# Kernel tuning notes

Measured on AMD Instinct MI355X. Metric: run time of the kernel, lower is better.

The kernel has to match this reference:

```python
import jax, jax.numpy as jnp
import numpy as np

B, D, H, NL, DFF, N = 64, 768, 12, 12, 3072, 197
HD = D // H  # 64
SCALE = HD ** -0.5


def setup_inputs() -> dict:
    key = jax.random.key(0)
    ks = iter(jax.random.split(key, 64))
    def rn(shape, s=0.02):
        return jax.random.normal(next(ks), shape, jnp.float32) * s
    inp = {
        'x': jax.random.normal(next(ks), (B, 12, 1000), jnp.float32),
        # PatchEmbed convs (torch Conv1d weight layout OIH)
        'conv1_w': rn((256, 12, 5), 0.1), 'conv1_b': jnp.zeros((256,), jnp.float32),
        'bn1_g': jnp.ones((256,), jnp.float32), 'bn1_b': jnp.zeros((256,), jnp.float32),
        'bn1_m': jnp.zeros((256,), jnp.float32), 'bn1_v': jnp.ones((256,), jnp.float32),
        'conv2_w': rn((768, 256, 5), 0.05), 'conv2_b': jnp.zeros((768,), jnp.float32),
        'bn2_g': jnp.ones((768,), jnp.float32), 'bn2_b': jnp.zeros((768,), jnp.float32),
        'bn2_m': jnp.zeros((768,), jnp.float32), 'bn2_v': jnp.ones((768,), jnp.float32),
        'cls_token': rn((1, 1, D)), 'pos_embed': rn((1, N, D)),
        # 12 transformer blocks, stacked. Linear weights stored [in, out].
        'ln1_g': jnp.ones((NL, D), jnp.float32), 'ln1_b': jnp.zeros((NL, D), jnp.float32),
        'qkv_w': rn((NL, D, 3 * D)),            # qkv_bias=False
        'proj_w': rn((NL, D, D)), 'proj_b': jnp.zeros((NL, D), jnp.float32),
        'ln2_g': jnp.ones((NL, D), jnp.float32), 'ln2_b': jnp.zeros((NL, D), jnp.float32),
        'fc1_w': rn((NL, D, DFF)), 'fc1_b': jnp.zeros((NL, DFF), jnp.float32),
        'fc2_w': rn((NL, DFF, D)), 'fc2_b': jnp.zeros((NL, D), jnp.float32),
        'norm_g': jnp.ones((D,), jnp.float32), 'norm_b': jnp.zeros((D,), jnp.float32),
        # ProjectionHead (nonlinear): Linear(768->768,no bias)+BN, ReLU, Linear(768->512,no bias)+BN
        'p1_w': rn((D, D)),
        'p1bn_g': jnp.ones((D,), jnp.float32), 'p1bn_b': jnp.zeros((D,), jnp.float32),
        'p1bn_m': jnp.zeros((D,), jnp.float32), 'p1bn_v': jnp.ones((D,), jnp.float32),
        'p2_w': rn((D, 512)),
        'p2bn_g': jnp.ones((512,), jnp.float32), 'p2bn_b': jnp.zeros((512,), jnp.float32),
        'p2bn_m': jnp.zeros((512,), jnp.float32), 'p2bn_v': jnp.ones((512,), jnp.float32),
    }
    return inp


def _conv1d(x, w, b, stride):
    y = jax.lax.conv_general_dilated(x, w, (stride,), 'VALID',
                                     dimension_numbers=('NCH', 'OIH', 'NCH'))
    return y + b[None, :, None]


def _bn_c(x, g, b, m, v, eps=1e-5):  # BatchNorm1d eval, channel axis 1 of (B,C,L)
    return (x - m[None, :, None]) * (g[None, :, None] / jnp.sqrt(v[None, :, None] + eps)) + b[None, :, None]


def _bn_f(x, g, b, m, v, eps=1e-5):  # BatchNorm1d eval on (B,F)
    return (x - m) * (g / jnp.sqrt(v + eps)) + b


def _ln(x, g, b, eps=1e-6):
    mu = x.mean(-1, keepdims=True)
    var = jnp.var(x, axis=-1, keepdims=True)
    return (x - mu) * jax.lax.rsqrt(var + eps) * g + b


def reference(x, conv1_w, conv1_b, bn1_g, bn1_b, bn1_m, bn1_v,
              conv2_w, conv2_b, bn2_g, bn2_b, bn2_m, bn2_v,
              cls_token, pos_embed,
              ln1_g, ln1_b, qkv_w, proj_w, proj_b,
              ln2_g, ln2_b, fc1_w, fc1_b, fc2_w, fc2_b,
              norm_g, norm_b,
              p1_w, p1bn_g, p1bn_b, p1bn_m, p1bn_v,
              p2_w, p2bn_g, p2bn_b, p2bn_m, p2bn_v):
    # PatchEmbed: conv -> ReLU -> BN, twice; then (B, 196, 768)
    h = _bn_c(jax.nn.relu(_conv1d(x, conv1_w, conv1_b, 5)), bn1_g, bn1_b, bn1_m, bn1_v)
    h = _bn_c(jax.nn.relu(_conv1d(h, conv2_w, conv2_b, 1)), bn2_g, bn2_b, bn2_m, bn2_v)
    h = jnp.transpose(h, (0, 2, 1))  # [B, 196, D]
    b = h.shape[0]
    tok = jnp.concatenate([jnp.broadcast_to(cls_token, (b, 1, D)), h], axis=1) + pos_embed  # [B, 197, D]

    for i in range(NL):
        y = _ln(tok, ln1_g[i], ln1_b[i])
        qkv = jnp.einsum('bnd,de->bne', y, qkv_w[i]).reshape(b, N, 3, H, HD)
        q, k, v = jnp.moveaxis(qkv, 2, 0)  # each [B, N, H, HD]
        q = jnp.transpose(q, (0, 2, 1, 3)) * SCALE  # [B, H, N, HD]
        k = jnp.transpose(k, (0, 2, 1, 3))
        v = jnp.transpose(v, (0, 2, 1, 3))
        attn = jax.nn.softmax(jnp.einsum('bhnd,bhmd->bhnm', q, k), axis=-1)
        o = jnp.einsum('bhnm,bhmd->bhnd', attn, v)
        o = jnp.transpose(o, (0, 2, 1, 3)).reshape(b, N, D)
        tok = tok + jnp.einsum('bnd,de->bne', o, proj_w[i]) + proj_b[i]
        y = _ln(tok, ln2_g[i], ln2_b[i])
        y = jax.nn.gelu(jnp.einsum('bnd,df->bnf', y, fc1_w[i]) + fc1_b[i], approximate=False)
        tok = tok + jnp.einsum('bnf,fd->bnd', y, fc2_w[i]) + fc2_b[i]

    cls = _ln(tok, norm_g, norm_b)[:, 0]  # global_pool='token'
    z = _bn_f(cls @ p1_w, p1bn_g, p1bn_b, p1bn_m, p1bn_v)
    z = jax.nn.relu(z)
    z = _bn_f(z @ p2_w, p2bn_g, p2bn_b, p2bn_m, p2bn_v)
    return z
```

## Files before the change

kernel.cpp:

```cpp
#include <hip/hip_runtime.h>
#include <hip/hip_bf16.h>

typedef __hip_bfloat16 bf16;
typedef __attribute__((ext_vector_type(8))) short bf16x8;
typedef __attribute__((ext_vector_type(4))) float f32x4;

__device__ __forceinline__ float bf2f(bf16 v) { return __bfloat162float(v); }
__device__ __forceinline__ unsigned short f2bfu(float f) {
    bf16 h = __float2bfloat16(f);
    return __builtin_bit_cast(unsigned short, h);
}

__device__ __forceinline__ void gload16(const void* g, void* lds) {
    __builtin_amdgcn_global_load_lds(
        (const __attribute__((address_space(1))) unsigned int*)g,
        (__attribute__((address_space(3))) unsigned int*)lds, 16, 0, 0);
}

__device__ __forceinline__ float gelu_f(float x) {
    float u = 0.7978845608f * (x + 0.044715f * x * x * x);
    float e = __expf(-2.0f * fabsf(u));
    float th = (1.f - e) / (1.f + e);
    th = u < 0.f ? -th : th;
    return 0.5f * x * (1.f + th);
}

__global__ __launch_bounds__(256)
void conv1_kernel(const float* __restrict__ x, const float* __restrict__ w,
                  const float* __restrict__ bias,
                  const float* __restrict__ g, const float* __restrict__ b,
                  const float* __restrict__ m, const float* __restrict__ v,
                  bf16* __restrict__ h1) {
    int bo = blockIdx.x;
    int bb = bo >> 8, o = bo & 255;
    int l = threadIdx.x;
    if (l >= 200) return;
    const float* wo = w + o * 60;
    const float* xb = x + bb * 12000;
    float acc = bias[o];
#pragma unroll
    for (int i = 0; i < 12; i++)
#pragma unroll
        for (int t = 0; t < 5; t++)
            acc = fmaf(xb[i * 1000 + 5 * l + t], wo[i * 5 + t], acc);
    acc = fmaxf(acc, 0.f);
    float sc = g[o] * rsqrtf(v[o] + 1e-5f);
    acc = (acc - m[o]) * sc + b[o];
    h1[bo * 200 + l] = __float2bfloat16(acc);
}

__global__ __launch_bounds__(256)
void im2col_kernel(const bf16* __restrict__ h1, bf16* __restrict__ A2) {
    int idx = blockIdx.x * 256 + threadIdx.x;
    int row = idx / 1280, c = idx - row * 1280;
    int bb = row / 196, l = row - bb * 196;
    int i = c / 5, t = c - i * 5;
    A2[idx] = h1[(bb * 256 + i) * 200 + l + t];
}

__global__ __launch_bounds__(256)
void add_cls_pos(const float* __restrict__ cls, const float* __restrict__ pos,
                 float* __restrict__ tok) {
    int idx = blockIdx.x * 256 + threadIdx.x;
    int bb = idx / 768, d = idx - bb * 768;
    tok[(size_t)bb * 197 * 768 + d] = cls[d] + pos[d];
}

__global__ __launch_bounds__(256)
void cvt_kernel(const float* __restrict__ in, bf16* __restrict__ out, int n) {
    int idx = blockIdx.x * 256 + threadIdx.x;
    if (idx < n) out[idx] = __float2bfloat16(in[idx]);
}

__global__ __launch_bounds__(256)
void wtrans_layer(const float* __restrict__ qkvw, const float* __restrict__ projw,
                  const float* __restrict__ fc1w, const float* __restrict__ fc2w,
                  bf16* __restrict__ qkvT, bf16* __restrict__ projT,
                  bf16* __restrict__ fc1T, bf16* __restrict__ fc2T) {
    __shared__ float tile[32][33];
    int blk = blockIdx.x;
    const float* in; bf16* out; int Kd, Nd, t0;
    if (blk < 1728)      { in = qkvw; out = qkvT; Kd = 768;  Nd = 2304; t0 = blk; }
    else if (blk < 2304) { in = projw; out = projT; Kd = 768;  Nd = 768;  t0 = blk - 1728; }
    else if (blk < 4608) { in = fc1w; out = fc1T; Kd = 768;  Nd = 3072; t0 = blk - 2304; }
    else                 { in = fc2w; out = fc2T; Kd = 3072; Nd = 768;  t0 = blk - 4608; }
    int ntiles = Nd >> 5;
    int kt = t0 / ntiles, nt = t0 - kt * ntiles;
    int k0 = kt * 32, n0 = nt * 32;
    int tx = threadIdx.x & 31, ty = threadIdx.x >> 5;
#pragma unroll
    for (int j = 0; j < 4; j++)
        tile[ty + 8 * j][tx] = in[(size_t)(k0 + ty + 8 * j) * Nd + n0 + tx];
    __syncthreads();
#pragma unroll
    for (int j = 0; j < 4; j++)
        out[(size_t)(n0 + ty + 8 * j) * Kd + k0 + tx] = __float2bfloat16(tile[tx][ty + 8 * j]);
}

__global__ __launch_bounds__(256)
void wtrans2(const float* __restrict__ in, bf16* __restrict__ out, int Kd, int Nd) {
    __shared__ float tile[32][33];
    int ntiles = Nd >> 5;
    int kt = blockIdx.x / ntiles, nt = blockIdx.x - kt * ntiles;
    int k0 = kt * 32, n0 = nt * 32;
    int tx = threadIdx.x & 31, ty = threadIdx.x >> 5;
#pragma unroll
    for (int j = 0; j < 4; j++)
        tile[ty + 8 * j][tx] = in[(size_t)(k0 + ty + 8 * j) * Nd + n0 + tx];
    __syncthreads();
#pragma unroll
    for (int j = 0; j < 4; j++)
        out[(size_t)(n0 + ty + 8 * j) * Kd + k0 + tx] = __float2bfloat16(tile[tx][ty + 8 * j]);
}

__global__ __launch_bounds__(256)
void ln_kernel(const float* __restrict__ x, bf16* __restrict__ y,
               const float* __restrict__ g, const float* __restrict__ b,
               int nrows, int xstride) {
    int row = blockIdx.x * 4 + (threadIdx.x >> 6);
    if (row >= nrows) return;
    int l = threadIdx.x & 63;
    const float* xr = x + (size_t)row * xstride;
    float4 v0 = *(const float4*)(xr + l * 4);
    float4 v1 = *(const float4*)(xr + 256 + l * 4);
    float4 v2 = *(const float4*)(xr + 512 + l * 4);
    float s1 = 0.f, s2 = 0.f;
    {
        float e;
        e = v0.x; s1 += e; s2 += e * e;  e = v0.y; s1 += e; s2 += e * e;
        e = v0.z; s1 += e; s2 += e * e;  e = v0.w; s1 += e; s2 += e * e;
        e = v1.x; s1 += e; s2 += e * e;  e = v1.y; s1 += e; s2 += e * e;
        e = v1.z; s1 += e; s2 += e * e;  e = v1.w; s1 += e; s2 += e * e;
        e = v2.x; s1 += e; s2 += e * e;  e = v2.y; s1 += e; s2 += e * e;
        e = v2.z; s1 += e; s2 += e * e;  e = v2.w; s1 += e; s2 += e * e;
    }
#pragma unroll
    for (int off = 1; off < 64; off <<= 1) {
        s1 += __shfl_xor(s1, off);
        s2 += __shfl_xor(s2, off);
    }
    float mu = s1 * (1.f / 768.f);
    float rs = rsqrtf(s2 * (1.f / 768.f) - mu * mu + 1e-6f);
    bf16* yr = y + (size_t)row * 768;
#pragma unroll
    for (int sgi = 0; sgi < 3; sgi++) {
        float4 vv = sgi == 0 ? v0 : (sgi == 1 ? v1 : v2);
        float4 gg = *(const float4*)(g + sgi * 256 + l * 4);
        float4 bb = *(const float4*)(b + sgi * 256 + l * 4);
        ushort4 o;
        o.x = f2bfu((vv.x - mu) * rs * gg.x + bb.x);
        o.y = f2bfu((vv.y - mu) * rs * gg.y + bb.y);
        o.z = f2bfu((vv.z - mu) * rs * gg.z + bb.z);
        o.w = f2bfu((vv.w - mu) * rs * gg.w + bb.w);
        *(ushort4*)(yr + sgi * 256 + l * 4) = o;
    }
}

enum { E_BF16 = 0, E_RESID = 1, E_GELU = 2, E_CONV2 = 3, E_HEAD1 = 4, E_HEAD2 = 5 };
#define GEMM_LDS 65536

template<int EPI>
__global__ __launch_bounds__(256)
void gemm2(const bf16* __restrict__ A, const bf16* __restrict__ Bt,
           int M, int N, int K,
           const float* __restrict__ bias,
           bf16* __restrict__ Co, float* __restrict__ tok,
           const float* __restrict__ bng, const float* __restrict__ bnb,
           const float* __restrict__ bnm, const float* __restrict__ bnv,
           const float* __restrict__ pos) {
    extern __shared__ char smem[];
    const int t = threadIdx.x;
    const int l = t & 63, w = t >> 6;
    const int wm = (w >> 1) * 64, wn = (w & 1) * 64;
    const int row0 = blockIdx.y * 128, col0 = blockIdx.x * 128;
    const int lr = l & 15, kg = l >> 4;

    const int srow = w * 8 + (l >> 3);
    const int sc = ((l & 7) ^ (l >> 3)) * 8;
    const int dstoff = w * 1024 + l * 16;

    const f32x4 zero4 = {0.f, 0.f, 0.f, 0.f};
    f32x4 acc[4][4];
#pragma unroll
    for (int i = 0; i < 4; i++)
#pragma unroll
        for (int j = 0; j < 4; j++) acc[i][j] = zero4;

    auto stage = [&](int b, int k0) {
#pragma unroll
        for (int p = 0; p < 4; p++) {
            int r = srow + p * 32;
            int gra = row0 + r; if (gra >= M) gra = M - 1;
            char* base = smem + b * 32768 + p * 4096 + dstoff;
            gload16(A + (size_t)gra * K + k0 + sc, base);
            gload16(Bt + (size_t)(col0 + r) * K + k0 + sc, base + 16384);
        }
    };

    const int nt = K >> 6;
    stage(0, 0);
    asm volatile("s_waitcnt vmcnt(0)" ::: "memory");
    __syncthreads();

    int cur = 0;
    for (int kt = 0; kt < nt; kt++) {
        if (kt + 1 < nt) stage(cur ^ 1, (kt + 1) << 6);
        const char* Ab = smem + cur * 32768;
        const char* Bb = Ab + 16384;
#pragma unroll
        for (int ks = 0; ks < 2; ks++) {
            bf16x8 af[4], bfv[4];
            const int cc = ((ks * 4 + kg) ^ (lr & 7)) * 16;
#pragma unroll
            for (int i = 0; i < 4; i++) {
                af[i]  = *(const bf16x8*)(Ab + (wm + i * 16 + lr) * 128 + cc);
                bfv[i] = *(const bf16x8*)(Bb + (wn + i * 16 + lr) * 128 + cc);
            }
#pragma unroll
            for (int i = 0; i < 4; i++)
#pragma unroll
                for (int j = 0; j < 4; j++)
                    acc[i][j] = __builtin_amdgcn_mfma_f32_16x16x32_bf16(af[i], bfv[j], acc[i][j], 0, 0, 0);
        }
        asm volatile("s_waitcnt vmcnt(0)" ::: "memory");
        __syncthreads();
        cur ^= 1;
    }

    const int rbase = row0 + wm + (kg << 2);
#pragma unroll
    for (int i = 0; i < 4; i++) {
#pragma unroll
        for (int sr = 0; sr < 4; sr++) {
            int r = rbase + i * 16 + sr;
            if (r < M) {
#pragma unroll
                for (int j = 0; j < 4; j++) {
                    int c = col0 + wn + j * 16 + lr;
                    float vv = acc[i][j][sr];
                    if (EPI == E_BF16) {
                        Co[(size_t)r * N + c] = __float2bfloat16(vv);
                    } else if (EPI == E_RESID) {
                        float* p = tok + (size_t)r * N + c;
                        *p += vv + bias[c];
                    } else if (EPI == E_GELU) {
                        Co[(size_t)r * N + c] = __float2bfloat16(gelu_f(vv + bias[c]));
                    } else if (EPI == E_CONV2) {
                        float xx = vv + bias[c];
                        xx = fmaxf(xx, 0.f);
                        float sc2 = bng[c] * rsqrtf(bnv[c] + 1e-5f);
                        xx = (xx - bnm[c]) * sc2 + bnb[c];
                        int bb = r / 196, ll = r - bb * 196;
                        xx += pos[(size_t)(1 + ll) * 768 + c];
                        tok[(size_t)(bb * 197 + 1 + ll) * 768 + c] = xx;
                    } else if (EPI == E_HEAD1) {
                        float sc2 = bng[c] * rsqrtf(bnv[c] + 1e-5f);
                        float xx = (vv - bnm[c]) * sc2 + bnb[c];
                        xx = fmaxf(xx, 0.f);
                        Co[(size_t)r * N + c] = __float2bfloat16(xx);
                    } else {
                        float sc2 = bng[c] * rsqrtf(bnv[c] + 1e-5f);
                        tok[(size_t)r * N + c] = (vv - bnm[c]) * sc2 + bnb[c];
                    }
                }
            }
        }
    }
}

#define ATTN_LDS (208 * 72 * 2 + 64 * 232 * 2 + 4 * 16 * 232 * 2)

__global__ __launch_bounds__(256)
void attn_kernel(const bf16* __restrict__ qkv, bf16* __restrict__ o) {
    extern __shared__ char smem[];
    bf16* Ks = (bf16*)smem;
    bf16* Vt = Ks + 208 * 72;
    bf16* Pl = Vt + 64 * 232;
    const int bh = blockIdx.x, bb = bh / 12, h = bh - bb * 12;
    const int t = threadIdx.x, w = t >> 6, l = t & 63;
    const int lr = l & 15, lk8 = (l >> 4) * 8;
    const size_t base = (size_t)bb * 197 * 2304 + (size_t)h * 64;

    for (int qi = t; qi < 197 * 16; qi += 256) {
        int n = qi >> 4, d4 = (qi & 15) << 2;
        ushort4 kv = *(const ushort4*)(qkv + base + (size_t)n * 2304 + 768 + d4);
        *(ushort4*)&Ks[n * 72 + d4] = kv;
    }
    for (int qi = t; qi < 11 * 72; qi += 256) ((unsigned short*)Ks)[197 * 72 + qi] = 0;
    for (int qi = t; qi < 197 * 16; qi += 256) {
        int n = qi >> 4, d4 = (qi & 15) << 2;
        ushort4 vv = *(const ushort4*)(qkv + base + (size_t)n * 2304 + 1536 + d4);
        ((unsigned short*)Vt)[(d4 + 0) * 232 + n] = vv.x;
        ((unsigned short*)Vt)[(d4 + 1) * 232 + n] = vv.y;
        ((unsigned short*)Vt)[(d4 + 2) * 232 + n] = vv.z;
        ((unsigned short*)Vt)[(d4 + 3) * 232 + n] = vv.w;
    }
    for (int qi = t; qi < 64 * 35; qi += 256) {
        int d = qi / 35, c = 197 + (qi - d * 35);
        ((unsigned short*)Vt)[d * 232 + c] = 0;
    }
    __syncthreads();

    bf16* Pw = Pl + w * (16 * 232);
    const f32x4 zero4 = {0.f, 0.f, 0.f, 0.f};
    for (int qt = w; qt < 13; qt += 4) {
        int m0 = qt * 16;
        int qrow = m0 + lr; if (qrow > 196) qrow = 196;
        const bf16* qp = qkv + (size_t)(bb * 197 + qrow) * 2304 + h * 64 + lk8;
        bf16x8 a0 = *(const bf16x8*)qp;
        bf16x8 a1 = *(const bf16x8*)(qp + 32);
        f32x4 s[13];
#pragma unroll
        for (int kt = 0; kt < 13; kt++) {
            const bf16* kp = &Ks[(kt * 16 + lr) * 72 + lk8];
            bf16x8 b0 = *(const bf16x8*)kp;
            bf16x8 b1 = *(const bf16x8*)(kp + 32);
            f32x4 z = zero4;
            z = __builtin_amdgcn_mfma_f32_16x16x32_bf16(a0, b0, z, 0, 0, 0);
            z = __builtin_amdgcn_mfma_f32_16x16x32_bf16(a1, b1, z, 0, 0, 0);
            s[kt] = z;
        }
        float mx[4] = {-1e30f, -1e30f, -1e30f, -1e30f};
#pragma unroll
        for (int kt = 0; kt < 13; kt++) {
            bool valid = (kt < 12) || (lr <= 4);
#pragma unroll
            for (int sr = 0; sr < 4; sr++) {
                float sv = s[kt][sr] * 0.125f;
                sv = valid ? sv : -1e30f;
                s[kt][sr] = sv;
                mx[sr] = fmaxf(mx[sr], sv);
            }
        }
#pragma unroll
        for (int off = 1; off < 16; off <<= 1)
#pragma unroll
            for (int sr = 0; sr < 4; sr++)
                mx[sr] = fmaxf(mx[sr], __shfl_xor(mx[sr], off));
        float sum[4] = {0.f, 0.f, 0.f, 0.f};
#pragma unroll
        for (int kt = 0; kt < 13; kt++)
#pragma unroll
            for (int sr = 0; sr < 4; sr++) {
                float p = __expf(s[kt][sr] - mx[sr]);
                s[kt][sr] = p;
                sum[sr] += p;
            }
#pragma unroll
        for (int off = 1; off < 16; off <<= 1)
#pragma unroll
            for (int sr = 0; sr < 4; sr++)
                sum[sr] += __shfl_xor(sum[sr], off);
        float inv[4];
#pragma unroll
        for (int sr = 0; sr < 4; sr++) inv[sr] = 1.f / sum[sr];
#pragma unroll
        for (int kt = 0; kt < 13; kt++)
#pragma unroll
            for (int sr = 0; sr < 4; sr++)
                ((unsigned short*)Pw)[((l >> 4) * 4 + sr) * 232 + kt * 16 + lr] =
                    f2bfu(s[kt][sr] * inv[sr]);
        for (int j = l; j < 256; j += 64) {
            int rr = j >> 4, cc = 208 + (j & 15);
            ((unsigned short*)Pw)[rr * 232 + cc] = 0;
        }
        asm volatile("s_waitcnt lgkmcnt(0)" ::: "memory");
        f32x4 oa[4];
#pragma unroll
        for (int nf = 0; nf < 4; nf++) oa[nf] = zero4;
#pragma unroll
        for (int ks = 0; ks < 7; ks++) {
            const bf16* pp = &Pw[lr * 232 + ks * 32 + lk8];
            bf16x8 ap = *(const bf16x8*)pp;
#pragma unroll
            for (int nf = 0; nf < 4; nf++) {
                bf16x8 bv = *(const bf16x8*)&Vt[(nf * 16 + lr) * 232 + ks * 32 + lk8];
                oa[nf] = __builtin_amdgcn_mfma_f32_16x16x32_bf16(ap, bv, oa[nf], 0, 0, 0);
            }
        }
#pragma unroll
        for (int nf = 0; nf < 4; nf++)
#pragma unroll
            for (int sr = 0; sr < 4; sr++) {
                int orow = m0 + (l >> 4) * 4 + sr;
                if (orow <= 196)
                    o[(size_t)(bb * 197 + orow) * 768 + h * 64 + nf * 16 + lr] =
                        __float2bfloat16(oa[nf][sr]);
            }
    }
}

extern "C" void kernel_launch(void* const* d_in, const int* in_sizes, int n_in,
                              void* d_out, int out_size, void* d_ws, size_t ws_size,
                              hipStream_t stream) {
    (void)in_sizes; (void)n_in; (void)out_size; (void)ws_size;
    const float* x        = (const float*)d_in[0];
    const float* conv1_w  = (const float*)d_in[1];
    const float* conv1_b  = (const float*)d_in[2];
    const float* bn1_g = (const float*)d_in[3],  *bn1_b = (const float*)d_in[4];
    const float* bn1_m = (const float*)d_in[5],  *bn1_v = (const float*)d_in[6];
    const float* conv2_w  = (const float*)d_in[7];
    const float* conv2_b  = (const float*)d_in[8];
    const float* bn2_g = (const float*)d_in[9],  *bn2_b = (const float*)d_in[10];
    const float* bn2_m = (const float*)d_in[11], *bn2_v = (const float*)d_in[12];
    const float* cls_tok  = (const float*)d_in[13];
    const float* pos      = (const float*)d_in[14];
    const float* ln1_g = (const float*)d_in[15], *ln1_b = (const float*)d_in[16];
    const float* qkv_w = (const float*)d_in[17];
    const float* proj_w = (const float*)d_in[18], *proj_b = (const float*)d_in[19];
    const float* ln2_g = (const float*)d_in[20], *ln2_b = (const float*)d_in[21];
    const float* fc1_w = (const float*)d_in[22], *fc1_b = (const float*)d_in[23];
    const float* fc2_w = (const float*)d_in[24], *fc2_b = (const float*)d_in[25];
    const float* norm_g = (const float*)d_in[26], *norm_b = (const float*)d_in[27];
    const float* p1_w = (const float*)d_in[28];
    const float* p1g = (const float*)d_in[29], *p1b = (const float*)d_in[30];
    const float* p1m = (const float*)d_in[31], *p1v = (const float*)d_in[32];
    const float* p2_w = (const float*)d_in[33];
    const float* p2g = (const float*)d_in[34], *p2b = (const float*)d_in[35];
    const float* p2m = (const float*)d_in[36], *p2v = (const float*)d_in[37];

    char* ws = (char*)d_ws;
    float* tok  = (float*)(ws + 0);
    bf16* ybf   = (bf16*)(ws + 38731776);
    bf16* qkvb  = (bf16*)(ws + 58097664);
    bf16* a1    = (bf16*)(ws + 116195328);
    bf16* h1    = (bf16*)(ws + 116195328);
    bf16* A2    = (bf16*)(ws + 116195328 + 8388608);
    bf16* clsb  = (bf16*)(ws + 193658880);
    bf16* z1    = (bf16*)(ws + 193757184);
    bf16* wtb   = (bf16*)(ws + 193953792);
    bf16* qkvT = wtb;
    bf16* projT = wtb + 1769472;
    bf16* fc1T = wtb + 2359296;
    bf16* fc2T = wtb + 4718592;
    bf16* conv2T = wtb;
    bf16* p1T = a1;
    bf16* p2T = a1 + 768 * 768;

    (void)hipFuncSetAttribute((const void*)attn_kernel,
                              hipFuncAttributeMaxDynamicSharedMemorySize, ATTN_LDS);
    (void)hipFuncSetAttribute((const void*)gemm2<E_BF16>,
                              hipFuncAttributeMaxDynamicSharedMemorySize, GEMM_LDS);
    (void)hipFuncSetAttribute((const void*)gemm2<E_RESID>,
                              hipFuncAttributeMaxDynamicSharedMemorySize, GEMM_LDS);
    (void)hipFuncSetAttribute((const void*)gemm2<E_GELU>,
                              hipFuncAttributeMaxDynamicSharedMemorySize, GEMM_LDS);
    (void)hipFuncSetAttribute((const void*)gemm2<E_CONV2>,
                              hipFuncAttributeMaxDynamicSharedMemorySize, GEMM_LDS);
    (void)hipFuncSetAttribute((const void*)gemm2<E_HEAD1>,
                              hipFuncAttributeMaxDynamicSharedMemorySize, GEMM_LDS);
    (void)hipFuncSetAttribute((const void*)gemm2<E_HEAD2>,
                              hipFuncAttributeMaxDynamicSharedMemorySize, GEMM_LDS);

    conv1_kernel<<<64 * 256, 256, 0, stream>>>(x, conv1_w, conv1_b, bn1_g, bn1_b, bn1_m, bn1_v, h1);
    im2col_kernel<<<(12544 * 1280) / 256, 256, 0, stream>>>(h1, A2);
    cvt_kernel<<<(768 * 1280 + 255) / 256, 256, 0, stream>>>(conv2_w, conv2T, 768 * 1280);
    gemm2<E_CONV2><<<dim3(6, 98), 256, GEMM_LDS, stream>>>(
        A2, conv2T, 12544, 768, 1280, conv2_b, nullptr, tok, bn2_g, bn2_b, bn2_m, bn2_v, pos);
    add_cls_pos<<<(64 * 768) / 256, 256, 0, stream>>>(cls_tok, pos, tok);

    const int MT = (12608 + 127) / 128;
    for (int i = 0; i < 12; i++) {
        wtrans_layer<<<6912, 256, 0, stream>>>(
            qkv_w + (size_t)i * 768 * 2304, proj_w + (size_t)i * 768 * 768,
            fc1_w + (size_t)i * 768 * 3072, fc2_w + (size_t)i * 3072 * 768,
            qkvT, projT, fc1T, fc2T);
        ln_kernel<<<12608 / 4, 256, 0, stream>>>(tok, ybf, ln1_g + i * 768, ln1_b + i * 768, 12608, 768);
        gemm2<E_BF16><<<dim3(18, MT), 256, GEMM_LDS, stream>>>(
            ybf, qkvT, 12608, 2304, 768,
            nullptr, qkvb, nullptr, nullptr, nullptr, nullptr, nullptr, nullptr);
        attn_kernel<<<768, 256, ATTN_LDS, stream>>>(qkvb, ybf);
        gemm2<E_RESID><<<dim3(6, MT), 256, GEMM_LDS, stream>>>(
            ybf, projT, 12608, 768, 768,
            proj_b + i * 768, nullptr, tok, nullptr, nullptr, nullptr, nullptr, nullptr);
        ln_kernel<<<12608 / 4, 256, 0, stream>>>(tok, ybf, ln2_g + i * 768, ln2_b + i * 768, 12608, 768);
        gemm2<E_GELU><<<dim3(24, MT), 256, GEMM_LDS, stream>>>(
            ybf, fc1T, 12608, 3072, 768,
            fc1_b + i * 3072, a1, nullptr, nullptr, nullptr, nullptr, nullptr, nullptr);
        gemm2<E_RESID><<<dim3(6, MT), 256, GEMM_LDS, stream>>>(
            a1, fc2T, 12608, 768, 3072,
            fc2_b + i * 768, nullptr, tok, nullptr, nullptr, nullptr, nullptr, nullptr);
    }

    ln_kernel<<<16, 256, 0, stream>>>(tok, clsb, norm_g, norm_b, 64, 197 * 768);
    wtrans2<<<576, 256, 0, stream>>>(p1_w, p1T, 768, 768);
    wtrans2<<<384, 256, 0, stream>>>(p2_w, p2T, 768, 512);
    gemm2<E_HEAD1><<<dim3(6, 1), 256, GEMM_LDS, stream>>>(
        clsb, p1T, 64, 768, 768,
        nullptr, z1, nullptr, p1g, p1b, p1m, p1v, nullptr);
    gemm2<E_HEAD2><<<dim3(4, 1), 256, GEMM_LDS, stream>>>(
        z1, p2T, 64, 512, 768,
        nullptr, nullptr, (float*)d_out, p2g, p2b, p2m, p2v, nullptr);
}
```

Before: 5.083 ms.

## Add 256x256 eight-wave GEMM for QKV and FC1 with XCD-aware block remap

Adds a new gemm8 kernel with 256x256 tiles, 512 threads and 128KB of LDS. It uses a four-phase half-tile pipeline with raw s_barrier, setprio and split waitcnts to overlap global-to-LDS loads with MFMA, and writes the output as packed bf16. The QKV and FC1 GEMMs now use this kernel, and both gemm kernels remap block IDs so consecutive tiles land on the same XCD for L2 reuse. The larger tiles cut operand reloads per FLOP, but they lower occupancy and leave more padding waste on the 12608-row M dimension.

```diff
diff --git a/kernel.cpp b/kernel.cpp
--- a/kernel.cpp
+++ b/kernel.cpp
@@ -172,7 +172,15 @@
     const int t = threadIdx.x;
     const int l = t & 63, w = t >> 6;
     const int wm = (w >> 1) * 64, wn = (w & 1) * 64;
-    const int row0 = blockIdx.y * 128, col0 = blockIdx.x * 128;
+
+    const int gx = gridDim.x;
+    const int nwg = gx * gridDim.y;
+    const int d = blockIdx.y * gx + blockIdx.x;
+    const int q = nwg >> 3, r = nwg & 7;
+    const int xcd = d & 7, pos_ = d >> 3;
+    const int lid = (xcd < r ? xcd * (q + 1) : r * (q + 1) + (xcd - r) * q) + pos_;
+    const int row0 = (lid / gx) * 128, col0 = (lid % gx) * 128;
+
     const int lr = l & 15, kg = l >> 4;
 
     const int srow = w * 8 + (l >> 3);
@@ -189,11 +197,11 @@
     auto stage = [&](int b, int k0) {
 #pragma unroll
         for (int p = 0; p < 4; p++) {
-            int r = srow + p * 32;
-            int gra = row0 + r; if (gra >= M) gra = M - 1;
+            int rr = srow + p * 32;
+            int gra = row0 + rr; if (gra >= M) gra = M - 1;
             char* base = smem + b * 32768 + p * 4096 + dstoff;
             gload16(A + (size_t)gra * K + k0 + sc, base);
-            gload16(Bt + (size_t)(col0 + r) * K + k0 + sc, base + 16384);
+            gload16(Bt + (size_t)(col0 + rr) * K + k0 + sc, base + 16384);
         }
     };
 
@@ -232,37 +240,165 @@
     for (int i = 0; i < 4; i++) {
 #pragma unroll
         for (int sr = 0; sr < 4; sr++) {
-            int r = rbase + i * 16 + sr;
-            if (r < M) {
+            int rr = rbase + i * 16 + sr;
+            if (rr < M) {
 #pragma unroll
                 for (int j = 0; j < 4; j++) {
                     int c = col0 + wn + j * 16 + lr;
                     float vv = acc[i][j][sr];
                     if (EPI == E_BF16) {
-                        Co[(size_t)r * N + c] = __float2bfloat16(vv);
+                        Co[(size_t)rr * N + c] = __float2bfloat16(vv);
                     } else if (EPI == E_RESID) {
-                        float* p = tok + (size_t)r * N + c;
+                        float* p = tok + (size_t)rr * N + c;
                         *p += vv + bias[c];
                     } else if (EPI == E_GELU) {
-                        Co[(size_t)r * N + c] = __float2bfloat16(gelu_f(vv + bias[c]));
+                        Co[(size_t)rr * N + c] = __float2bfloat16(gelu_f(vv + bias[c]));
                     } else if (EPI == E_CONV2) {
                         float xx = vv + bias[c];
                         xx = fmaxf(xx, 0.f);
                         float sc2 = bng[c] * rsqrtf(bnv[c] + 1e-5f);
                         xx = (xx - bnm[c]) * sc2 + bnb[c];
-                        int bb = r / 196, ll = r - bb * 196;
+                        int bb = rr / 196, ll = rr - bb * 196;
                         xx += pos[(size_t)(1 + ll) * 768 + c];
                         tok[(size_t)(bb * 197 + 1 + ll) * 768 + c] = xx;
                     } else if (EPI == E_HEAD1) {
                         float sc2 = bng[c] * rsqrtf(bnv[c] + 1e-5f);
                         float xx = (vv - bnm[c]) * sc2 + bnb[c];
                         xx = fmaxf(xx, 0.f);
-                        Co[(size_t)r * N + c] = __float2bfloat16(xx);
+                        Co[(size_t)rr * N + c] = __float2bfloat16(xx);
                     } else {
                         float sc2 = bng[c] * rsqrtf(bnv[c] + 1e-5f);
-                        tok[(size_t)r * N + c] = (vv - bnm[c]) * sc2 + bnb[c];
+                        tok[(size_t)rr * N + c] = (vv - bnm[c]) * sc2 + bnb[c];
                     }
                 }
+            }
+        }
+    }
+}
+
+#define G8_LDS 131072
+
+#define G8_PHASE(PH, TILE, DOSTAGE, VM)                                              \
+    {                                                                                \
+        const int kh_ = (PH) >> 1, mh_ = (PH) & 1;                                   \
+        const char* bufb = smem + (((TILE) & 1) * 65536) + kh_ * 32768;              \
+        bf16x8 afr[4], bfr[4];                                                       \
+        _Pragma("unroll") for (int n = 0; n < 4; ++n)                                \
+            bfr[n] = *(const bf16x8*)(bufb + boff + n * 1024);                       \
+        _Pragma("unroll") for (int fi = 0; fi < 4; ++fi)                             \
+            afr[fi] = *(const bf16x8*)(bufb + aoff + mh_ * 4096 + fi * 1024);        \
+        if (DOSTAGE) stageH(PH, (TILE) + 1);                                         \
+        if ((VM) == 4) asm volatile("s_waitcnt vmcnt(4)" ::: "memory");              \
+        if ((VM) == 0) asm volatile("s_waitcnt vmcnt(0)" ::: "memory");              \
+        __builtin_amdgcn_sched_barrier(0);                                           \
+        __builtin_amdgcn_s_barrier();                                                \
+        __builtin_amdgcn_sched_barrier(0);                                           \
+        asm volatile("s_waitcnt lgkmcnt(0)" ::: "memory");                           \
+        __builtin_amdgcn_sched_barrier(0);                                           \
+        __builtin_amdgcn_s_setprio(1);                                               \
+        _Pragma("unroll") for (int fi = 0; fi < 4; ++fi)                             \
+            _Pragma("unroll") for (int n = 0; n < 4; ++n)                            \
+                acc[mh_ * 4 + fi][n] = __builtin_amdgcn_mfma_f32_16x16x32_bf16(      \
+                    bfr[n], afr[fi], acc[mh_ * 4 + fi][n], 0, 0, 0);                 \
+        __builtin_amdgcn_s_setprio(0);                                               \
+        __builtin_amdgcn_sched_barrier(0);                                           \
+        __builtin_amdgcn_s_barrier();                                                \
+        __builtin_amdgcn_sched_barrier(0);                                           \
+    }
+
+template<int EPI>
+__global__ __launch_bounds__(512, 2)
+void gemm8(const bf16* __restrict__ A, const bf16* __restrict__ Bt,
+           int M, int N, int K,
+           const float* __restrict__ bias, bf16* __restrict__ Co) {
+    extern __shared__ char smem[];
+    const int t = threadIdx.x;
+    const int l = t & 63, wid = t >> 6;
+    const int wr = wid >> 2, wc = wid & 3;
+    const int lr = l & 15, kg = l >> 4;
+
+    const int gx = gridDim.x;
+    const int nwg = gx * gridDim.y;
+    const int d = blockIdx.y * gx + blockIdx.x;
+    const int q = nwg >> 3, r = nwg & 7;
+    const int xcd = d & 7, pp = d >> 3;
+    const int lid = (xcd < r ? xcd * (q + 1) : r * (q + 1) + (xcd - r) * q) + pp;
+    const int row0 = (lid / gx) * 256, col0 = (lid % gx) * 256;
+
+    const int srow = wid * 32 + (l >> 2);
+    const int schunk = ((l & 3) ^ ((l >> 2) & 3)) * 8;
+    int gra0 = row0 + srow;      if (gra0 >= M) gra0 = M - 1;
+    int gra1 = row0 + srow + 16; if (gra1 >= M) gra1 = M - 1;
+    const bf16* ApS0 = A + (size_t)gra0 * K + schunk;
+    const bf16* ApS1 = A + (size_t)gra1 * K + schunk;
+    const bf16* BpS0 = Bt + (size_t)(col0 + srow) * K + schunk;
+    const bf16* BpS1 = Bt + (size_t)(col0 + srow + 16) * K + schunk;
+    const int sdst = wid * 2048 + l * 16;
+
+    const f32x4 zero4 = {0.f, 0.f, 0.f, 0.f};
+    f32x4 acc[8][4];
+#pragma unroll
+    for (int i = 0; i < 8; i++)
+#pragma unroll
+        for (int n = 0; n < 4; n++) acc[i][n] = zero4;
+
+    auto stageH = [&](int h, int tile) {
+        char* hb = smem + ((tile & 1) * 65536) + h * 16384 + sdst;
+        const int ko = tile * 64 + (h >> 1) * 32;
+        if ((h & 1) == 0) { gload16(ApS0 + ko, hb); gload16(ApS1 + ko, hb + 1024); }
+        else              { gload16(BpS0 + ko, hb); gload16(BpS1 + ko, hb + 1024); }
+    };
+
+    const int ccr = (kg ^ (lr & 3)) * 16;
+    const int aoff = (wr * 128 + lr) * 64 + ccr;
+    const int boff = 16384 + (wc * 64 + lr) * 64 + ccr;
+
+    const int nt = K >> 6;
+#pragma unroll
+    for (int h = 0; h < 4; ++h) stageH(h, 0);
+    asm volatile("s_waitcnt vmcnt(4)" ::: "memory");
+    __builtin_amdgcn_sched_barrier(0);
+    __builtin_amdgcn_s_barrier();
+    __builtin_amdgcn_sched_barrier(0);
+
+    for (int T = 0; T < nt - 1; ++T) {
+        G8_PHASE(0, T, true, -1)
+        G8_PHASE(1, T, true, 4)
+        G8_PHASE(2, T, true, -1)
+        G8_PHASE(3, T, true, 4)
+    }
+    G8_PHASE(0, nt - 1, false, -1)
+    G8_PHASE(1, nt - 1, false, 0)
+    G8_PHASE(2, nt - 1, false, -1)
+    G8_PHASE(3, nt - 1, false, -1)
+
+    const int rbl = row0 + wr * 128 + lr;
+    const int cb0 = col0 + wc * 64 + kg * 4;
+    float bsv[4][4];
+    if (EPI == E_GELU) {
+#pragma unroll
+        for (int n = 0; n < 4; ++n)
+#pragma unroll
+            for (int sr = 0; sr < 4; ++sr)
+                bsv[n][sr] = bias[cb0 + n * 16 + sr];
+    }
+#pragma unroll
+    for (int i = 0; i < 8; ++i) {
+        int rr = rbl + i * 16;
+        if (rr < M) {
+            bf16* op = Co + (size_t)rr * N + cb0;
+#pragma unroll
+            for (int n = 0; n < 4; ++n) {
+                float v0 = acc[i][n][0], v1 = acc[i][n][1];
+                float v2 = acc[i][n][2], v3 = acc[i][n][3];
+                if (EPI == E_GELU) {
+                    v0 = gelu_f(v0 + bsv[n][0]); v1 = gelu_f(v1 + bsv[n][1]);
+                    v2 = gelu_f(v2 + bsv[n][2]); v3 = gelu_f(v3 + bsv[n][3]);
+                }
+                uint2 pk;
+                pk.x = (unsigned)f2bfu(v0) | ((unsigned)f2bfu(v1) << 16);
+                pk.y = (unsigned)f2bfu(v2) | ((unsigned)f2bfu(v3) << 16);
+                *(uint2*)(op + n * 16) = pk;
             }
         }
     }
@@ -439,18 +575,18 @@
 
     (void)hipFuncSetAttribute((const void*)attn_kernel,
                               hipFuncAttributeMaxDynamicSharedMemorySize, ATTN_LDS);
-    (void)hipFuncSetAttribute((const void*)gemm2<E_BF16>,
+    (void)hipFuncSetAttribute((const void*)gemm2<E_CONV2>,
                               hipFuncAttributeMaxDynamicSharedMemorySize, GEMM_LDS);
     (void)hipFuncSetAttribute((const void*)gemm2<E_RESID>,
-                              hipFuncAttributeMaxDynamicSharedMemorySize, GEMM_LDS);
-    (void)hipFuncSetAttribute((const void*)gemm2<E_GELU>,
-                              hipFuncAttributeMaxDynamicSharedMemorySize, GEMM_LDS);
-    (void)hipFuncSetAttribute((const void*)gemm2<E_CONV2>,
                               hipFuncAttributeMaxDynamicSharedMemorySize, GEMM_LDS);
     (void)hipFuncSetAttribute((const void*)gemm2<E_HEAD1>,
                               hipFuncAttributeMaxDynamicSharedMemorySize, GEMM_LDS);
     (void)hipFuncSetAttribute((const void*)gemm2<E_HEAD2>,
                               hipFuncAttributeMaxDynamicSharedMemorySize, GEMM_LDS);
+    (void)hipFuncSetAttribute((const void*)gemm8<E_BF16>,
+                              hipFuncAttributeMaxDynamicSharedMemorySize, G8_LDS);
+    (void)hipFuncSetAttribute((const void*)gemm8<E_GELU>,
+                              hipFuncAttributeMaxDynamicSharedMemorySize, G8_LDS);
 
     conv1_kernel<<<64 * 256, 256, 0, stream>>>(x, conv1_w, conv1_b, bn1_g, bn1_b, bn1_m, bn1_v, h1);
     im2col_kernel<<<(12544 * 1280) / 256, 256, 0, stream>>>(h1, A2);
@@ -460,23 +596,22 @@
     add_cls_pos<<<(64 * 768) / 256, 256, 0, stream>>>(cls_tok, pos, tok);
 
     const int MT = (12608 + 127) / 128;
+    const int MT3 = (12608 + 255) / 256;
     for (int i = 0; i < 12; i++) {
         wtrans_layer<<<6912, 256, 0, stream>>>(
             qkv_w + (size_t)i * 768 * 2304, proj_w + (size_t)i * 768 * 768,
             fc1_w + (size_t)i * 768 * 3072, fc2_w + (size_t)i * 3072 * 768,
             qkvT, projT, fc1T, fc2T);
         ln_kernel<<<12608 / 4, 256, 0, stream>>>(tok, ybf, ln1_g + i * 768, ln1_b + i * 768, 12608, 768);
-        gemm2<E_BF16><<<dim3(18, MT), 256, GEMM_LDS, stream>>>(
-            ybf, qkvT, 12608, 2304, 768,
-            nullptr, qkvb, nullptr, nullptr, nullptr, nullptr, nullptr, nullptr);
+        gemm8<E_BF16><<<dim3(9, MT3), 512, G8_LDS, stream>>>(
+            ybf, qkvT, 12608, 2304, 768, nullptr, qkvb);
         attn_kernel<<<768, 256, ATTN_LDS, stream>>>(qkvb, ybf);
         gemm2<E_RESID><<<dim3(6, MT), 256, GEMM_LDS, stream>>>(
             ybf, projT, 12608, 768, 768,
             proj_b + i * 768, nullptr, tok, nullptr, nullptr, nullptr, nullptr, nullptr);
         ln_kernel<<<12608 / 4, 256, 0, stream>>>(tok, ybf, ln2_g + i * 768, ln2_b + i * 768, 12608, 768);
-        gemm2<E_GELU><<<dim3(24, MT), 256, GEMM_LDS, stream>>>(
-            ybf, fc1T, 12608, 3072, 768,
-            fc1_b + i * 3072, a1, nullptr, nullptr, nullptr, nullptr, nullptr, nullptr);
+        gemm8<E_GELU><<<dim3(12, MT3), 512, G8_LDS, stream>>>(
+            ybf, fc1T, 12608, 3072, 768, fc1_b + i * 3072, a1);
         gemm2<E_RESID><<<dim3(6, MT), 256, GEMM_LDS, stream>>>(
             a1, fc2T, 12608, 768, 3072,
             fc2_b + i * 768, nullptr, tok, nullptr, nullptr, nullptr, nullptr, nullptr);
```

Result: no change. 5.012 ms (-1.4%).
